# Kernel tuning notes

Hardware: AMD Instinct MI355X
Metric: run time of the kernel (lower is better)

## Reference

```python
import jax, jax.numpy as jnp
import numpy as np
from jax import lax

B, C, H = 64, 3, 224
F = 8  # number of 3x3 filters
POOL = (H - 2) // 2  # 111
FEAT = POOL * POOL * F  # 98568


def setup_inputs() -> dict:
    key = jax.random.key(0)
    ks = jax.random.split(key, 8)
    return {
        "x": jax.random.normal(ks[0], (B, C, H, H), dtype=jnp.float32),
        "filters": jax.random.normal(ks[1], (F, 3, 3), dtype=jnp.float32),
        "W1": jax.random.normal(ks[2], (FEAT, 512), dtype=jnp.float32) * 0.01,
        "b1": jax.random.normal(ks[3], (512,), dtype=jnp.float32) * 0.01,
        "W2": jax.random.normal(ks[4], (512, 256), dtype=jnp.float32) * 0.02,
        "b2": jax.random.normal(ks[5], (256,), dtype=jnp.float32) * 0.02,
        "Wo": jax.random.normal(ks[6], (256, 1000), dtype=jnp.float32) * 0.02,
        "bo": jax.random.normal(ks[7], (1000,), dtype=jnp.float32) * 0.02,
    }


def reference(x, filters, W1, b1, W2, b2, Wo, bo):
    # conv_r + conv_g + conv_b == conv(r+g+b, filt) by linearity -> sum channels once
    s = x.sum(axis=1, keepdims=True)  # [B,1,H,H]
    k = filters[:, None, :, :]  # [F,1,3,3] (OIHW)
    conv = lax.conv_general_dilated(
        s, k, window_strides=(1, 1), padding="VALID",
        dimension_numbers=("NCHW", "OIHW", "NCHW"))  # [B,F,222,222]
    conv = jax.nn.relu(conv)
    pooled = lax.reduce_window(
        conv, -jnp.inf, lax.max,
        window_dimensions=(1, 1, 2, 2), window_strides=(1, 1, 2, 2),
        padding="VALID")  # [B,F,111,111]
    flat = pooled.reshape(x.shape[0], -1)  # filter-major layout matches torch cat order
    h = jax.nn.relu(flat @ W1 + b1)
    h = jax.nn.relu(h @ W2 + b2)
    return jax.nn.softmax(h @ Wo + bo, axis=1)
```

## Files before the change

### kernel.cpp

```cpp
#include <hip/hip_runtime.h>
#include <math.h>

#define Bsz 64
#define Himg 224
#define HS (Himg*Himg)
#define PW 111
#define PP (PW*PW)
#define Fn 8
#define FEAT (Fn*PP)
#define FEATP 98592
#define KC 32
#define NT32_TOT 3081
#define NCH 192
#define N1 512
#define N2 256
#define N3 1000
#define RG 8

typedef short short8 __attribute__((ext_vector_type(8)));
typedef float f32x4 __attribute__((ext_vector_type(4)));

#define GLOAD_LDS16(g, l)                                                     \
  __builtin_amdgcn_global_load_lds(                                           \
      (const __attribute__((address_space(1))) void*)(g),                     \
      (__attribute__((address_space(3))) void*)(l), 16, 0, 0)

__device__ __forceinline__ void cvt_hilo(const float* v, short8& hi, short8& lo) {
#pragma unroll
  for (int j = 0; j < 8; j++) {
    unsigned u = __builtin_bit_cast(unsigned, v[j]);
    hi[j] = (short)(u >> 16);
    float hf = __builtin_bit_cast(float, u & 0xFFFF0000u);
    float r = v[j] - hf;
    lo[j] = (short)(__builtin_bit_cast(unsigned, r) >> 16);
  }
}

__global__ void k_convpool(const float* __restrict__ x, const float* __restrict__ filt,
                           short* __restrict__ Ah, short* __restrict__ Al) {
  int i = blockIdx.x * 256 + threadIdx.x;
  if (i < Bsz * (FEATP - FEAT)) {
    size_t pidx = (size_t)(i / 24) * FEATP + FEAT + (i % 24);
    Ah[pidx] = 0; Al[pidx] = 0;
  }
  if (i >= Bsz * PP) return;
  int b = i / PP, r = i - b * PP;
  int py = r / PW, px = r - py * PW;
  const float* xb = x + (size_t)b * 3 * HS + (size_t)(2 * py) * Himg + 2 * px;
  float p[4][4];
#pragma unroll
  for (int dy = 0; dy < 4; dy++) {
    const float* row = xb + dy * Himg;
    float2 a0 = *(const float2*)(row);
    float2 a1 = *(const float2*)(row + 2);
    float2 b0 = *(const float2*)(row + HS);
    float2 b1 = *(const float2*)(row + HS + 2);
    float2 c0 = *(const float2*)(row + 2 * HS);
    float2 c1 = *(const float2*)(row + 2 * HS + 2);
    p[dy][0] = a0.x + b0.x + c0.x;
    p[dy][1] = a0.y + b0.y + c0.y;
    p[dy][2] = a1.x + b1.x + c1.x;
    p[dy][3] = a1.y + b1.y + c1.y;
  }
  size_t base = (size_t)b * FEATP + r;
#pragma unroll
  for (int f = 0; f < Fn; f++) {
    float mx = 0.f;
#pragma unroll
    for (int oy = 0; oy < 2; oy++)
#pragma unroll
      for (int ox = 0; ox < 2; ox++) {
        float c = 0.f;
#pragma unroll
        for (int dy = 0; dy < 3; dy++)
#pragma unroll
          for (int dx = 0; dx < 3; dx++)
            c = fmaf(p[oy + dy][ox + dx], filt[f * 9 + dy * 3 + dx], c);
        mx = fmaxf(mx, c);
      }
    unsigned u = __builtin_bit_cast(unsigned, mx);
    float hf = __builtin_bit_cast(float, u & 0xFFFF0000u);
    float rr = mx - hf;
    Ah[base + (size_t)f * PP] = (short)(u >> 16);
    Al[base + (size_t)f * PP] = (short)(__builtin_bit_cast(unsigned, rr) >> 16);
  }
}

__global__ void __launch_bounds__(256) k_gemm1(const short* __restrict__ Ah,
                                               const short* __restrict__ Al,
                                               const float* __restrict__ W,
                                               float* __restrict__ partial) {
  __shared__ float Wl[2][KC][128];
  __shared__ short Ashi[2][64 * 32];
  __shared__ short Aslo[2][64 * 32];
  const int t = threadIdx.x;
  const int wv = t >> 6;
  const int lane = t & 63;
  const int wgid = blockIdx.x;
  const int nid = (wgid & 7) * 96 + (wgid >> 3);
  const int col0b = (nid & 3) * 128;
  const int c = nid >> 2;
  const int tile0 = c * 16 + min(c, 9);
  const int nt = (c < 9) ? 17 : 16;
  const int lrow = lane & 15;
  const int lg8 = (lane >> 4) * 8;
  const int wsr = lane >> 5;
  const int wscx = ((lane & 31) * 4) ^ ((wv & 1) << 4);
  const int wcol = wv * 32 + lrow;
  const int wcolsw = wcol ^ (((lg8 >> 3) & 1) << 4);
  const size_t aoff = (size_t)(wv * 16 + (lane >> 2)) * FEATP + (lane & 3) * 8;

  f32x4 acc[4][2];
#pragma unroll
  for (int mf = 0; mf < 4; mf++)
#pragma unroll
    for (int nf = 0; nf < 2; nf++)
#pragma unroll
      for (int r = 0; r < 4; r++) acc[mf][nf][r] = 0.f;

#define STAGE_W(buf, kt)                                                      \
  {                                                                           \
    const int kb = (kt) * KC + wv * 8;                                        \
    _Pragma("unroll")                                                         \
    for (int p = 0; p < 4; p++) {                                             \
      int krow = kb + 2 * p + wsr;                                            \
      krow = krow < FEAT ? krow : FEAT - 1;       \
      GLOAD_LDS16(W + (size_t)krow * N1 + col0b + wscx,                       \
                  &Wl[buf][wv * 8 + 2 * p][0]);                               \
    }                                                                         \
  }
#define STAGE_A(buf, kt)                                                      \
  {                                                                           \
    const int kb = (kt) * KC;                                                 \
    GLOAD_LDS16(Ah + aoff + kb, &Ashi[buf][wv * 16 * 32]);                    \
    GLOAD_LDS16(Al + aoff + kb, &Aslo[buf][wv * 16 * 32]);                    \
  }

  STAGE_W(0, tile0)
  STAGE_A(0, tile0)
  __syncthreads();

  for (int s = 0; s < nt; s++) {
    const int buf = s & 1;
    const bool more = (s + 1) < nt;
    if (more) {
      STAGE_W(buf ^ 1, tile0 + s + 1)
      STAGE_A(buf ^ 1, tile0 + s + 1)
    }
    float bv0[8], bv1[8];
#pragma unroll
    for (int j = 0; j < 8; j++) {
      bv0[j] = Wl[buf][lg8 + j][wcolsw];
      bv1[j] = Wl[buf][lg8 + j][wcolsw ^ 16];
    }
    short8 bhi[2], blo[2];
    cvt_hilo(bv0, bhi[0], blo[0]);
    cvt_hilo(bv1, bhi[1], blo[1]);
#pragma unroll
    for (int mf = 0; mf < 4; mf++) {
      const int r = mf * 16 + lrow;
      short8 ahi = *(const short8*)&Ashi[buf][r * 32 + lg8];
      short8 alo = *(const short8*)&Aslo[buf][r * 32 + lg8];
#pragma unroll
      for (int nf = 0; nf < 2; nf++) {
        acc[mf][nf] = __builtin_amdgcn_mfma_f32_16x16x32_bf16(ahi, bhi[nf], acc[mf][nf], 0, 0, 0);
        acc[mf][nf] = __builtin_amdgcn_mfma_f32_16x16x32_bf16(ahi, blo[nf], acc[mf][nf], 0, 0, 0);
        acc[mf][nf] = __builtin_amdgcn_mfma_f32_16x16x32_bf16(alo, bhi[nf], acc[mf][nf], 0, 0, 0);
      }
    }
    __syncthreads();
  }

  const int drow = (lane >> 4) * 4;
#pragma unroll
  for (int mf = 0; mf < 4; mf++) {
#pragma unroll
    for (int nf = 0; nf < 2; nf++) {
      float* pp = partial + ((size_t)c * Bsz + mf * 16 + drow) * N1 +
                  col0b + wv * 32 + nf * 16 + lrow;
#pragma unroll
      for (int r = 0; r < 4; r++) pp[(size_t)r * N1] = acc[mf][nf][r];
    }
  }
}

__global__ void k_red1a(const float4* __restrict__ partial, float4* __restrict__ partial2) {
  int i = blockIdx.x * 256 + threadIdx.x;
  int g = blockIdx.y;
  int c0 = g * 24;
  const int Q = Bsz * N1 / 4;
  float4 s = make_float4(0.f, 0.f, 0.f, 0.f);
#pragma unroll 4
  for (int c = c0; c < c0 + 24; c++) {
    float4 v = partial[(size_t)c * Q + i];
    s.x += v.x; s.y += v.y; s.z += v.z; s.w += v.w;
  }
  partial2[(size_t)g * Q + i] = s;
}

__global__ void __launch_bounds__(256) k_gemm2(const float* __restrict__ partial2,
                                               const float* __restrict__ b1,
                                               const float* __restrict__ W2,
                                               const float* __restrict__ b2,
                                               float* __restrict__ h2) {
  const int m = blockIdx.x >> 2;
  const int nq = blockIdx.x & 3;
  const int t = threadIdx.x;
  __shared__ float a[N1];
  __shared__ float red[4][64];
#pragma unroll
  for (int e = 0; e < 2; e++) {
    int idx = e * 256 + t;
    float sum = 0.f;
#pragma unroll
    for (int g = 0; g < RG; g++)
      sum += partial2[(size_t)g * Bsz * N1 + (size_t)m * N1 + idx];
    a[idx] = fmaxf(sum + b1[idx], 0.f);
  }
  __syncthreads();
  const int col = nq * 64 + (t & 63);
  const int ks = (t >> 6) * 128;
  float sum = 0.f;
#pragma unroll 8
  for (int k = 0; k < 128; k++)
    sum = fmaf(a[ks + k], W2[(size_t)(ks + k) * N2 + col], sum);
  red[t >> 6][t & 63] = sum;
  __syncthreads();
  if (t < 64) {
    float tot = red[0][t] + red[1][t] + red[2][t] + red[3][t] + b2[nq * 64 + t];
    h2[(size_t)m * N2 + nq * 64 + t] = fmaxf(tot, 0.f);
  }
}

__global__ void __launch_bounds__(256) k_logits(const float* __restrict__ h2,
                                                const float* __restrict__ Wo,
                                                const float* __restrict__ bo,
                                                float* __restrict__ logits) {
  const int m = blockIdx.x >> 2;
  const int nc = blockIdx.x & 3;
  const int t = threadIdx.x;
  __shared__ float a[N2];
  a[t] = h2[(size_t)m * N2 + t];
  __syncthreads();
  const int col = nc * 250 + t;
  if (t >= 250) return;
  float sum = bo[col];
#pragma unroll 8
  for (int k = 0; k < N2; k++)
    sum = fmaf(a[k], Wo[(size_t)k * N3 + col], sum);
  logits[(size_t)m * N3 + col] = sum;
}

__global__ void __launch_bounds__(256) k_softmax(const float* __restrict__ logits,
                                                 float* __restrict__ out) {
  const int m = blockIdx.x;
  const int t = threadIdx.x;
  __shared__ float red[8];
  float vals[4];
  float vmax = -3.4e38f;
#pragma unroll
  for (int j = 0; j < 4; j++) {
    int n = j * 256 + t;
    vals[j] = (n < N3) ? logits[(size_t)m * N3 + n] : -3.4e38f;
    vmax = fmaxf(vmax, vals[j]);
  }
#pragma unroll
  for (int off = 32; off > 0; off >>= 1) vmax = fmaxf(vmax, __shfl_xor(vmax, off));
  const int wid = t >> 6;
  if ((t & 63) == 0) red[wid] = vmax;
  __syncthreads();
  vmax = fmaxf(fmaxf(red[0], red[1]), fmaxf(red[2], red[3]));
  float ev[4];
  float esum = 0.f;
#pragma unroll
  for (int j = 0; j < 4; j++) {
    int n = j * 256 + t;
    float e = (n < N3) ? __expf(vals[j] - vmax) : 0.f;
    ev[j] = e;
    esum += e;
  }
#pragma unroll
  for (int off = 32; off > 0; off >>= 1) esum += __shfl_xor(esum, off);
  if ((t & 63) == 0) red[4 + wid] = esum;
  __syncthreads();
  esum = red[4] + red[5] + red[6] + red[7];
  float inv = 1.f / esum;
#pragma unroll
  for (int j = 0; j < 4; j++) {
    int n = j * 256 + t;
    if (n < N3) out[(size_t)m * N3 + n] = ev[j] * inv;
  }
}

extern "C" void kernel_launch(void* const* d_in, const int* in_sizes, int n_in,
                              void* d_out, int out_size, void* d_ws, size_t ws_size,
                              hipStream_t stream) {
  const float* x = (const float*)d_in[0];
  const float* filters = (const float*)d_in[1];
  const float* W1 = (const float*)d_in[2];
  const float* b1 = (const float*)d_in[3];
  const float* W2 = (const float*)d_in[4];
  const float* b2 = (const float*)d_in[5];
  const float* Wo = (const float*)d_in[6];
  const float* bo = (const float*)d_in[7];
  float* out = (float*)d_out;

  short* Ah = (short*)d_ws;
  short* Al = Ah + (size_t)Bsz * FEATP;
  float* partial = (float*)(Al + (size_t)Bsz * FEATP);
  float* partial2 = partial + (size_t)NCH * Bsz * N1;
  float* h2 = partial2 + (size_t)RG * Bsz * N1;
  float* logits = h2 + (size_t)Bsz * N2;

  k_convpool<<<(Bsz * PP + 255) / 256, 256, 0, stream>>>(x, filters, Ah, Al);
  k_gemm1<<<4 * NCH, 256, 0, stream>>>(Ah, Al, W1, partial);
  dim3 gr(Bsz * N1 / 4 / 256, RG);
  k_red1a<<<gr, 256, 0, stream>>>((const float4*)partial, (float4*)partial2);
  k_gemm2<<<Bsz * 4, 256, 0, stream>>>(partial2, b1, W2, b2, h2);
  k_logits<<<Bsz * 4, 256, 0, stream>>>(h2, Wo, bo, logits);
  k_softmax<<<Bsz, 256, 0, stream>>>(logits, out);
}
```

Baseline: 93.87 us.

## Swizzle A-tile LDS layout and collapse split-K reduction into one pass

The global source offset for the A tile staging is XOR-swizzled per row, and the MFMA-side LDS reads use the matching swizzle. The aim is to spread the short8 A reads across LDS banks and cut bank conflicts. The two-stage split-K reduction (k_red1a plus the partial2 sum inside k_gemm2) becomes a single k_red kernel that sums all 192 chunks, adds bias and applies ReLU into h1. That removes one intermediate buffer and the reduce work inside k_gemm2, but the new kernel uses scalar loads over fewer blocks, so it keeps less memory traffic in flight.

```diff
diff --git a/kernel.cpp b/kernel.cpp
--- a/kernel.cpp
+++ b/kernel.cpp
@@ -15,7 +15,6 @@
 #define N1 512
 #define N2 256
 #define N3 1000
-#define RG 8
 
 typedef short short8 __attribute__((ext_vector_type(8)));
 typedef float f32x4 __attribute__((ext_vector_type(4)));
@@ -108,7 +107,9 @@
   const int wscx = ((lane & 31) * 4) ^ ((wv & 1) << 4);
   const int wcol = wv * 32 + lrow;
   const int wcolsw = wcol ^ (((lg8 >> 3) & 1) << 4);
-  const size_t aoff = (size_t)(wv * 16 + (lane >> 2)) * FEATP + (lane & 3) * 8;
+  const int arl = lane >> 2;
+  const int ags = (lane & 3) ^ ((arl >> 1) & 3);
+  const size_t aoff = (size_t)(wv * 16 + arl) * FEATP + ags * 8;
 
   f32x4 acc[4][2];
 #pragma unroll
@@ -158,9 +159,10 @@
     cvt_hilo(bv1, bhi[1], blo[1]);
 #pragma unroll
     for (int mf = 0; mf < 4; mf++) {
-      const int r = mf * 16 + lrow;
-      short8 ahi = *(const short8*)&Ashi[buf][r * 32 + lg8];
-      short8 alo = *(const short8*)&Aslo[buf][r * 32 + lg8];
+      const int rr = mf * 16 + lrow;
+      const int gq = ((lane >> 4) ^ ((rr >> 1) & 3)) * 8;
+      short8 ahi = *(const short8*)&Ashi[buf][rr * 32 + gq];
+      short8 alo = *(const short8*)&Aslo[buf][rr * 32 + gq];
 #pragma unroll
       for (int nf = 0; nf < 2; nf++) {
         acc[mf][nf] = __builtin_amdgcn_mfma_f32_16x16x32_bf16(ahi, bhi[nf], acc[mf][nf], 0, 0, 0);
@@ -184,22 +186,16 @@
   }
 }
 
-__global__ void k_red1a(const float4* __restrict__ partial, float4* __restrict__ partial2) {
+__global__ void k_red(const float* __restrict__ partial, const float* __restrict__ b1,
+                      float* __restrict__ h1) {
   int i = blockIdx.x * 256 + threadIdx.x;
-  int g = blockIdx.y;
-  int c0 = g * 24;
-  const int Q = Bsz * N1 / 4;
-  float4 s = make_float4(0.f, 0.f, 0.f, 0.f);
-#pragma unroll 4
-  for (int c = c0; c < c0 + 24; c++) {
-    float4 v = partial[(size_t)c * Q + i];
-    s.x += v.x; s.y += v.y; s.z += v.z; s.w += v.w;
-  }
-  partial2[(size_t)g * Q + i] = s;
-}
-
-__global__ void __launch_bounds__(256) k_gemm2(const float* __restrict__ partial2,
-                                               const float* __restrict__ b1,
+  float sum = 0.f;
+#pragma unroll 8
+  for (int c = 0; c < NCH; c++) sum += partial[(size_t)c * Bsz * N1 + i];
+  h1[i] = fmaxf(sum + b1[i & (N1 - 1)], 0.f);
+}
+
+__global__ void __launch_bounds__(256) k_gemm2(const float* __restrict__ h1,
                                                const float* __restrict__ W2,
                                                const float* __restrict__ b2,
                                                float* __restrict__ h2) {
@@ -208,15 +204,8 @@
   const int t = threadIdx.x;
   __shared__ float a[N1];
   __shared__ float red[4][64];
-#pragma unroll
-  for (int e = 0; e < 2; e++) {
-    int idx = e * 256 + t;
-    float sum = 0.f;
-#pragma unroll
-    for (int g = 0; g < RG; g++)
-      sum += partial2[(size_t)g * Bsz * N1 + (size_t)m * N1 + idx];
-    a[idx] = fmaxf(sum + b1[idx], 0.f);
-  }
+  a[t] = h1[(size_t)m * N1 + t];
+  a[256 + t] = h1[(size_t)m * N1 + 256 + t];
   __syncthreads();
   const int col = nq * 64 + (t & 63);
   const int ks = (t >> 6) * 128;
@@ -308,15 +297,14 @@
   short* Ah = (short*)d_ws;
   short* Al = Ah + (size_t)Bsz * FEATP;
   float* partial = (float*)(Al + (size_t)Bsz * FEATP);
-  float* partial2 = partial + (size_t)NCH * Bsz * N1;
-  float* h2 = partial2 + (size_t)RG * Bsz * N1;
+  float* h1 = partial + (size_t)NCH * Bsz * N1;
+  float* h2 = h1 + (size_t)Bsz * N1;
   float* logits = h2 + (size_t)Bsz * N2;
 
   k_convpool<<<(Bsz * PP + 255) / 256, 256, 0, stream>>>(x, filters, Ah, Al);
   k_gemm1<<<4 * NCH, 256, 0, stream>>>(Ah, Al, W1, partial);
-  dim3 gr(Bsz * N1 / 4 / 256, RG);
-  k_red1a<<<gr, 256, 0, stream>>>((const float4*)partial, (float4*)partial2);
-  k_gemm2<<<Bsz * 4, 256, 0, stream>>>(partial2, b1, W2, b2, h2);
+  k_red<<<Bsz * N1 / 256, 256, 0, stream>>>(partial, b1, h1);
+  k_gemm2<<<Bsz * 4, 256, 0, stream>>>(h1, W2, b2, h2);
   k_logits<<<Bsz * 4, 256, 0, stream>>>(h2, Wo, bo, logits);
   k_softmax<<<Bsz, 256, 0, stream>>>(logits, out);
 }
```

Measured after the change: 98.71 us. 5.2% more time.
